# Kernel tuning notes

Measured on AMD Instinct MI355X. Metric: run time of the kernel, lower is better.

## Reference

```python
import jax, jax.numpy as jnp
import numpy as np

DIM = 384
HEADS = 6
K = 3  # kernel_size, stride = 1


def setup_inputs() -> dict:
    key = jax.random.key(0)
    ks = jax.random.split(key, 7)
    B, H, W, C = 16, 56, 56, DIM
    sc = 1.0 / np.sqrt(C)
    return {
        "x_map": jax.random.normal(ks[0], (B, H, W, C), dtype=jnp.float32),
        # Linear weights stored [in, out] (torch stores [out, in]; math identical)
        "W_attn": jax.random.normal(ks[1], (C, HEADS * K * K), dtype=jnp.float32) * sc,
        "b_attn": jax.random.normal(ks[2], (HEADS * K * K,), dtype=jnp.float32) * 0.02,
        "W_v": jax.random.normal(ks[3], (C, C), dtype=jnp.float32) * sc,
        "b_v": jax.random.normal(ks[4], (C,), dtype=jnp.float32) * 0.02,
        "W_proj": jax.random.normal(ks[5], (C, C), dtype=jnp.float32) * sc,
        "b_proj": jax.random.normal(ks[6], (C,), dtype=jnp.float32) * 0.02,
    }


def reference(x_map, W_attn, b_attn, W_v, b_v, W_proj, b_proj):
    B, H, W, C = x_map.shape
    k, heads = K, HEADS
    hd = C // heads
    pad = k // 2

    # attention logits per output pixel: [B, H*W, heads, k*k], softmax over window
    a = x_map @ W_attn + b_attn                     # [B,H,W,heads*k*k]
    a = jax.nn.softmax(a.reshape(B, H * W, heads, k * k), axis=-1)

    v = x_map @ W_v + b_v                           # [B,H,W,C]
    vp = jnp.pad(v, ((0, 0), (pad, pad), (pad, pad), (0, 0)))
    # k*k shifted views == F.unfold with row-major (ki,kj) kernel order
    patches = jnp.stack(
        [vp[:, i:i + H, j:j + W, :] for i in range(k) for j in range(k)],
        axis=3,
    )                                               # [B,H,W,k*k,C]
    patches = patches.reshape(B, H * W, k * k, heads, hd)

    # softmax-weighted sum over the k*k window, per head
    y = jnp.einsum('bpKhd,bphK->bphd', patches, a)  # [B,H*W,heads,hd]
    y = y.reshape(B, H, W, C)
    return y @ W_proj + b_proj
```

## Files before the change

### kernel.cpp

```cpp
#include <hip/hip_runtime.h>
#include <math.h>

#define NPIX 50176
#define CDIM 384
#define HEADS 6
#define NLOGIT 54
#define HH 56
#define WW 56
#define NCAT 448

typedef __attribute__((ext_vector_type(8))) __bf16 bf16x8;
typedef __attribute__((ext_vector_type(4))) float f32x4;

__device__ __forceinline__ void glds16(const void* g, void* l) {
  __builtin_amdgcn_global_load_lds(
      (const __attribute__((address_space(1))) unsigned int*)g,
      (__attribute__((address_space(3))) unsigned int*)l, 16, 0, 0);
}

__global__ __launch_bounds__(256) void prep_kernel(
    const float* __restrict__ W_v, const float* __restrict__ W_proj,
    const float* __restrict__ W_attn, const float* __restrict__ b_attn,
    __bf16* __restrict__ Wcat, __bf16* __restrict__ Wtp,
    float* __restrict__ bpad) {
  const int idx = blockIdx.x * 256 + threadIdx.x;
  const int CATSZ = NCAT * CDIM;
  const int WSZ   = CDIM * CDIM;
  if (idx < CATSZ) {
    const int n = idx / CDIM, k = idx % CDIM;
    float val;
    if (n < CDIM) val = W_v[k * CDIM + n];
    else {
      const int nn = n - CDIM;
      val = (nn < NLOGIT) ? W_attn[k * NLOGIT + nn] : 0.f;
    }
    Wcat[idx] = (__bf16)val;
  } else if (idx < CATSZ + WSZ) {
    const int r = idx - CATSZ;
    const int n = r / CDIM, k = r % CDIM;
    Wtp[r] = (__bf16)W_proj[k * CDIM + n];
  } else if (idx < CATSZ + WSZ + 64) {
    const int n = idx - CATSZ - WSZ;
    bpad[n] = (n < NLOGIT) ? b_attn[n] : 0.f;
  }
}

__global__ __launch_bounds__(256) void gemm_v_logit_kernel(
    const float* __restrict__ X, const __bf16* __restrict__ Wcat,
    const float* __restrict__ b_v, __bf16* __restrict__ v,
    const float* __restrict__ bpad, float* __restrict__ attn) {
  __shared__ char smem[33792];
  __bf16 (*As)[40] = (__bf16(*)[40])smem;
  __bf16 (*Bs)[32] = (__bf16(*)[32])(smem + 5120);
  float (*Ls)[68]  = (float(*)[68])smem;

  const int tid  = threadIdx.x;
  const int wave = tid >> 6;
  const int lane = tid & 63;
  const int bm   = blockIdx.x * 64;
  const int srow  = lane >> 2;
  const int skoff = (lane & 3) * 8;
  const int frow  = lane & 15;
  const int fk    = (lane >> 4) * 8;
  const size_t xrow = (size_t)(bm + wave * 16 + srow) * CDIM;

  f32x4 acc[28] = {};

  float4 pa0 = *(const float4*)(X + xrow + skoff);
  float4 pa1 = *(const float4*)(X + xrow + skoff + 4);

  for (int ks = 0; ks < 12; ++ks) {
    const int k0 = ks * 32;
    #pragma unroll
    for (int c = 0; c < 7; ++c) {
      const int brow = wave * 112 + c * 16;
      glds16(Wcat + (size_t)(brow + srow) * CDIM + k0 + skoff, &Bs[brow][0]);
    }
    bf16x8 h;
    h[0] = (__bf16)pa0.x; h[1] = (__bf16)pa0.y; h[2] = (__bf16)pa0.z; h[3] = (__bf16)pa0.w;
    h[4] = (__bf16)pa1.x; h[5] = (__bf16)pa1.y; h[6] = (__bf16)pa1.z; h[7] = (__bf16)pa1.w;
    *(bf16x8*)&As[wave * 16 + srow][skoff] = h;
    if (ks < 11) {
      pa0 = *(const float4*)(X + xrow + k0 + 32 + skoff);
      pa1 = *(const float4*)(X + xrow + k0 + 36 + skoff);
    }
    __syncthreads();

    const bf16x8 a = *(const bf16x8*)&As[wave * 16 + frow][fk];
    #pragma unroll
    for (int ni = 0; ni < 28; ++ni) {
      const bf16x8 b = *(const bf16x8*)&Bs[ni * 16 + frow][fk];
      acc[ni] = __builtin_amdgcn_mfma_f32_16x16x32_bf16(a, b, acc[ni], 0, 0, 0);
    }
    __syncthreads();
  }

  const int orow = (lane >> 4) * 4;

  #pragma unroll
  for (int ni = 0; ni < 24; ++ni) {
    const int n = ni * 16 + frow;
    const float bvl = b_v[n];
    #pragma unroll
    for (int r = 0; r < 4; ++r) {
      const int m = bm + wave * 16 + orow + r;
      v[(size_t)m * CDIM + n] = (__bf16)(acc[ni][r] + bvl);
    }
  }

  float bvl[4];
  #pragma unroll
  for (int ni = 0; ni < 4; ++ni) bvl[ni] = bpad[ni * 16 + frow];
  #pragma unroll
  for (int ni = 0; ni < 4; ++ni)
    #pragma unroll
    for (int r = 0; r < 4; ++r)
      Ls[wave * 16 + orow + r][ni * 16 + frow] = acc[24 + ni][r] + bvl[ni];
  __syncthreads();

  #pragma unroll
  for (int it = 0; it < 2; ++it) {
    const int task = it * 256 + tid;
    if (task < 64 * HEADS) {
      const int pl = task / HEADS;
      const int h  = task % HEADS;
      const float* row = &Ls[pl][h * 9];
      float m = row[0];
      #pragma unroll
      for (int w = 1; w < 9; ++w) m = fmaxf(m, row[w]);
      float e[9], s = 0.f;
      #pragma unroll
      for (int w = 0; w < 9; ++w) { e[w] = __expf(row[w] - m); s += e[w]; }
      const float inv = 1.f / s;
      float* op = &attn[(size_t)(bm + pl) * NLOGIT + h * 9];
      #pragma unroll
      for (int w = 0; w < 9; ++w) op[w] = e[w] * inv;
    }
  }
}

__global__ __launch_bounds__(256) void gemm_proj_kernel(
    const __bf16* __restrict__ A, const __bf16* __restrict__ Bt,
    const float* __restrict__ bias, float* __restrict__ Out) {
  __shared__ __bf16 As[64][32];
  __shared__ __bf16 Bs[384][32];

  const int tid  = threadIdx.x;
  const int wave = tid >> 6;
  const int lane = tid & 63;
  const int bm   = blockIdx.x * 64;
  const int srow  = lane >> 2;
  const int skoff = (lane & 3) * 8;
  const int frow  = lane & 15;
  const int fk    = (lane >> 4) * 8;

  f32x4 acc[24] = {};

  for (int ks = 0; ks < 12; ++ks) {
    const int k0 = ks * 32;
    glds16(A + (size_t)(bm + wave * 16 + srow) * CDIM + k0 + skoff,
           &As[wave * 16][0]);
    #pragma unroll
    for (int c = 0; c < 6; ++c) {
      const int brow = wave * 96 + c * 16;
      glds16(Bt + (size_t)(brow + srow) * CDIM + k0 + skoff, &Bs[brow][0]);
    }
    __syncthreads();

    const bf16x8 a = *(const bf16x8*)&As[wave * 16 + frow][fk];
    #pragma unroll
    for (int ni = 0; ni < 24; ++ni) {
      const bf16x8 b = *(const bf16x8*)&Bs[ni * 16 + frow][fk];
      acc[ni] = __builtin_amdgcn_mfma_f32_16x16x32_bf16(a, b, acc[ni], 0, 0, 0);
    }
    __syncthreads();
  }

  const int orow = (lane >> 4) * 4;
  #pragma unroll
  for (int ni = 0; ni < 24; ++ni) {
    const int n = ni * 16 + frow;
    const float bvl = bias[n];
    #pragma unroll
    for (int r = 0; r < 4; ++r) {
      const int m = bm + wave * 16 + orow + r;
      Out[(size_t)m * CDIM + n] = acc[ni][r] + bvl;
    }
  }
}

__global__ __launch_bounds__(256) void aggregate_kernel(
    const __bf16* __restrict__ v, const float* __restrict__ attn,
    __bf16* __restrict__ y) {
  const int idx = blockIdx.x * 256 + threadIdx.x;
  const int cg = idx % 48;
  const int pg = idx / 48;
  const int c  = cg * 8;
  const int b  = pg / ((HH / 4) * WW);
  const int r2 = pg % ((HH / 4) * WW);
  const int i0 = (r2 / WW) * 4;
  const int j  = r2 % WW;
  const int head = c >> 6;

  const int pbase = (b * HH + i0) * WW + j;
  float aw[4][9];
  #pragma unroll
  for (int p = 0; p < 4; ++p) {
    const float* ap = attn + (size_t)(pbase + p * WW) * NLOGIT + head * 9;
    #pragma unroll
    for (int w = 0; w < 9; ++w) aw[p][w] = ap[w];
  }

  const bool j0ok = (j > 0), j2ok = (j < WW - 1);
  float acc[4][8] = {};

  #pragma unroll
  for (int li = 0; li < 6; ++li) {
    const int ii = i0 - 1 + li;
    if (ii < 0 || ii >= HH) continue;
    const __bf16* vrow = v + ((size_t)(b * HH + ii) * WW + j) * CDIM + c;
    float ch[3][8];
    #pragma unroll
    for (int kj = 0; kj < 3; ++kj) {
      const bool ok = (kj == 0) ? j0ok : (kj == 2) ? j2ok : true;
      if (ok) {
        const bf16x8 vv = *(const bf16x8*)(vrow + (kj - 1) * CDIM);
        #pragma unroll
        for (int q = 0; q < 8; ++q) ch[kj][q] = (float)vv[q];
      } else {
        #pragma unroll
        for (int q = 0; q < 8; ++q) ch[kj][q] = 0.f;
      }
    }
    #pragma unroll
    for (int p = 0; p < 4; ++p) {
      const int ki = li - p;
      if (ki < 0 || ki > 2) continue;
      #pragma unroll
      for (int kj = 0; kj < 3; ++kj) {
        const float w = aw[p][ki * 3 + kj];
        #pragma unroll
        for (int q = 0; q < 8; ++q) acc[p][q] += w * ch[kj][q];
      }
    }
  }

  #pragma unroll
  for (int p = 0; p < 4; ++p) {
    bf16x8 o;
    #pragma unroll
    for (int q = 0; q < 8; ++q) o[q] = (__bf16)acc[p][q];
    *(bf16x8*)&y[(size_t)(pbase + p * WW) * CDIM + c] = o;
  }
}

extern "C" void kernel_launch(void* const* d_in, const int* in_sizes, int n_in,
                              void* d_out, int out_size, void* d_ws,
                              size_t ws_size, hipStream_t stream) {
  const float* x      = (const float*)d_in[0];
  const float* W_attn = (const float*)d_in[1];
  const float* b_attn = (const float*)d_in[2];
  const float* W_v    = (const float*)d_in[3];
  const float* b_v    = (const float*)d_in[4];
  const float* W_proj = (const float*)d_in[5];
  const float* b_proj = (const float*)d_in[6];
  float* out = (float*)d_out;

  char* w = (char*)d_ws;
  __bf16* v    = (__bf16*)w;  w += (size_t)NPIX * CDIM * 2;
  __bf16* y    = (__bf16*)w;  w += (size_t)NPIX * CDIM * 2;
  float*  attn = (float*)w;   w += (size_t)NPIX * NLOGIT * 4;
  __bf16* Wcat = (__bf16*)w;  w += (size_t)NCAT * CDIM * 2;
  __bf16* Wtp  = (__bf16*)w;  w += (size_t)CDIM * CDIM * 2;
  float*  bpad = (float*)w;   w += 64 * 4;

  const int prep_n = NCAT * CDIM + CDIM * CDIM + 64;
  prep_kernel<<<(prep_n + 255) / 256, 256, 0, stream>>>(
      W_v, W_proj, W_attn, b_attn, Wcat, Wtp, bpad);

  gemm_v_logit_kernel<<<NPIX / 64, 256, 0, stream>>>(
      x, Wcat, b_v, v, bpad, attn);

  aggregate_kernel<<<(NPIX / 4 * 48) / 256, 256, 0, stream>>>(v, attn, y);

  gemm_proj_kernel<<<NPIX / 64, 256, 0, stream>>>(y, Wtp, b_proj, out);
}
```

Measured before the change: 119.4 us.

## Pre-swizzle weights into MFMA fragment order and load A operands directly to registers

The prep kernel now writes both bf16 weight matrices in per-lane MFMA fragment order, so each k-step's B tile is a contiguous block copied straight into LDS and read back with linear, conflict-free 16-byte reads. The A operand (X or y) is loaded directly from global memory into registers in fragment layout, dropping the A shared-memory tile and its LDS round trip. The y load in the projection GEMM is prefetched one step ahead. The trade-off is that each lane's A loads now cover 16 distinct rows rather than coalesced row segments, which may reduce global coalescing.

Result: no change. 118.1 us (-1.1%).

```diff
diff --git a/kernel.cpp b/kernel.cpp
--- a/kernel.cpp
+++ b/kernel.cpp
@@ -8,6 +8,9 @@
 #define HH 56
 #define WW 56
 #define NCAT 448
+#define KSTEPS 12
+#define NCH_V 28
+#define NCH_P 24
 
 typedef __attribute__((ext_vector_type(8))) __bf16 bf16x8;
 typedef __attribute__((ext_vector_type(4))) float f32x4;
@@ -21,75 +24,90 @@
 __global__ __launch_bounds__(256) void prep_kernel(
     const float* __restrict__ W_v, const float* __restrict__ W_proj,
     const float* __restrict__ W_attn, const float* __restrict__ b_attn,
-    __bf16* __restrict__ Wcat, __bf16* __restrict__ Wtp,
+    __bf16* __restrict__ Wcat_frag, __bf16* __restrict__ Wtp_frag,
     float* __restrict__ bpad) {
-  const int idx = blockIdx.x * 256 + threadIdx.x;
-  const int CATSZ = NCAT * CDIM;
-  const int WSZ   = CDIM * CDIM;
-  if (idx < CATSZ) {
-    const int n = idx / CDIM, k = idx % CDIM;
-    float val;
-    if (n < CDIM) val = W_v[k * CDIM + n];
-    else {
-      const int nn = n - CDIM;
-      val = (nn < NLOGIT) ? W_attn[k * NLOGIT + nn] : 0.f;
-    }
-    Wcat[idx] = (__bf16)val;
-  } else if (idx < CATSZ + WSZ) {
-    const int r = idx - CATSZ;
-    const int n = r / CDIM, k = r % CDIM;
-    Wtp[r] = (__bf16)W_proj[k * CDIM + n];
-  } else if (idx < CATSZ + WSZ + 64) {
-    const int n = idx - CATSZ - WSZ;
+  const int gid = blockIdx.x * 256 + threadIdx.x;
+  const int NV = KSTEPS * NCH_V * 64;
+  const int NP = KSTEPS * NCH_P * 64;
+  if (gid < NV) {
+    const int ks   = gid / (NCH_V * 64);
+    const int rem  = gid % (NCH_V * 64);
+    const int ni   = rem >> 6;
+    const int lane = rem & 63;
+    const int n  = ni * 16 + (lane & 15);
+    const int kb = ks * 32 + (lane >> 4) * 8;
+    bf16x8 o;
+    #pragma unroll
+    for (int q = 0; q < 8; ++q) {
+      const int k = kb + q;
+      float val;
+      if (n < CDIM) val = W_v[k * CDIM + n];
+      else {
+        const int nn = n - CDIM;
+        val = (nn < NLOGIT) ? W_attn[k * NLOGIT + nn] : 0.f;
+      }
+      o[q] = (__bf16)val;
+    }
+    *(bf16x8*)&Wcat_frag[(size_t)gid * 8] = o;
+  } else if (gid < NV + NP) {
+    const int r    = gid - NV;
+    const int ks   = r / (NCH_P * 64);
+    const int rem  = r % (NCH_P * 64);
+    const int ni   = rem >> 6;
+    const int lane = rem & 63;
+    const int n  = ni * 16 + (lane & 15);
+    const int kb = ks * 32 + (lane >> 4) * 8;
+    bf16x8 o;
+    #pragma unroll
+    for (int q = 0; q < 8; ++q) o[q] = (__bf16)W_proj[(kb + q) * CDIM + n];
+    *(bf16x8*)&Wtp_frag[(size_t)r * 8] = o;
+  } else if (gid < NV + NP + 64) {
+    const int n = gid - NV - NP;
     bpad[n] = (n < NLOGIT) ? b_attn[n] : 0.f;
   }
 }
 
 __global__ __launch_bounds__(256) void gemm_v_logit_kernel(
-    const float* __restrict__ X, const __bf16* __restrict__ Wcat,
+    const float* __restrict__ X, const __bf16* __restrict__ Wcat_frag,
     const float* __restrict__ b_v, __bf16* __restrict__ v,
     const float* __restrict__ bpad, float* __restrict__ attn) {
-  __shared__ char smem[33792];
-  __bf16 (*As)[40] = (__bf16(*)[40])smem;
-  __bf16 (*Bs)[32] = (__bf16(*)[32])(smem + 5120);
-  float (*Ls)[68]  = (float(*)[68])smem;
+  __shared__ char smem[NCH_V * 1024];
+  __bf16* Bs = (__bf16*)smem;
+  float (*Ls)[68] = (float(*)[68])smem;
 
   const int tid  = threadIdx.x;
   const int wave = tid >> 6;
   const int lane = tid & 63;
   const int bm   = blockIdx.x * 64;
-  const int srow  = lane >> 2;
-  const int skoff = (lane & 3) * 8;
-  const int frow  = lane & 15;
-  const int fk    = (lane >> 4) * 8;
-  const size_t xrow = (size_t)(bm + wave * 16 + srow) * CDIM;
+  const int frow = lane & 15;
+  const int fk8  = (lane >> 4) * 8;
+
+  const int arow = bm + wave * 16 + frow;
+  const float* xrow = X + (size_t)arow * CDIM + fk8;
 
   f32x4 acc[28] = {};
-
-  float4 pa0 = *(const float4*)(X + xrow + skoff);
-  float4 pa1 = *(const float4*)(X + xrow + skoff + 4);
-
-  for (int ks = 0; ks < 12; ++ks) {
-    const int k0 = ks * 32;
+  float4 pa0 = *(const float4*)(xrow + 0);
+  float4 pa1 = *(const float4*)(xrow + 4);
+
+  for (int ks = 0; ks < KSTEPS; ++ks) {
     #pragma unroll
     for (int c = 0; c < 7; ++c) {
-      const int brow = wave * 112 + c * 16;
-      glds16(Wcat + (size_t)(brow + srow) * CDIM + k0 + skoff, &Bs[brow][0]);
-    }
-    bf16x8 h;
-    h[0] = (__bf16)pa0.x; h[1] = (__bf16)pa0.y; h[2] = (__bf16)pa0.z; h[3] = (__bf16)pa0.w;
-    h[4] = (__bf16)pa1.x; h[5] = (__bf16)pa1.y; h[6] = (__bf16)pa1.z; h[7] = (__bf16)pa1.w;
-    *(bf16x8*)&As[wave * 16 + srow][skoff] = h;
-    if (ks < 11) {
-      pa0 = *(const float4*)(X + xrow + k0 + 32 + skoff);
-      pa1 = *(const float4*)(X + xrow + k0 + 36 + skoff);
+      const int chunk = wave * 7 + c;
+      glds16(Wcat_frag + ((size_t)(ks * NCH_V + chunk) * 64 + lane) * 8,
+             Bs + chunk * 512);
+    }
+    bf16x8 a;
+    a[0] = (__bf16)pa0.x; a[1] = (__bf16)pa0.y; a[2] = (__bf16)pa0.z; a[3] = (__bf16)pa0.w;
+    a[4] = (__bf16)pa1.x; a[5] = (__bf16)pa1.y; a[6] = (__bf16)pa1.z; a[7] = (__bf16)pa1.w;
+    if (ks < KSTEPS - 1) {
+      pa0 = *(const float4*)(xrow + (ks + 1) * 32 + 0);
+      pa1 = *(const float4*)(xrow + (ks + 1) * 32 + 4);
     }
     __syncthreads();
 
-    const bf16x8 a = *(const bf16x8*)&As[wave * 16 + frow][fk];
     #pragma unroll
     for (int ni = 0; ni < 28; ++ni) {
-      const bf16x8 b = *(const bf16x8*)&Bs[ni * 16 + frow][fk];
+      const bf16x8 b = *(const bf16x8*)&Bs[(ni * 64 + lane) * 8];
       acc[ni] = __builtin_amdgcn_mfma_f32_16x16x32_bf16(a, b, acc[ni], 0, 0, 0);
     }
     __syncthreads();
@@ -140,40 +158,41 @@
 }
 
 __global__ __launch_bounds__(256) void gemm_proj_kernel(
-    const __bf16* __restrict__ A, const __bf16* __restrict__ Bt,
+    const __bf16* __restrict__ Y, const __bf16* __restrict__ Wtp_frag,
     const float* __restrict__ bias, float* __restrict__ Out) {
-  __shared__ __bf16 As[64][32];
-  __shared__ __bf16 Bs[384][32];
+  __shared__ __bf16 Bs[NCH_P * 512];
 
   const int tid  = threadIdx.x;
   const int wave = tid >> 6;
   const int lane = tid & 63;
   const int bm   = blockIdx.x * 64;
-  const int srow  = lane >> 2;
-  const int skoff = (lane & 3) * 8;
-  const int frow  = lane & 15;
-  const int fk    = (lane >> 4) * 8;
+  const int frow = lane & 15;
+  const int fk8  = (lane >> 4) * 8;
+
+  const int arow = bm + wave * 16 + frow;
+  const __bf16* yrow = Y + (size_t)arow * CDIM + fk8;
 
   f32x4 acc[24] = {};
-
-  for (int ks = 0; ks < 12; ++ks) {
-    const int k0 = ks * 32;
-    glds16(A + (size_t)(bm + wave * 16 + srow) * CDIM + k0 + skoff,
-           &As[wave * 16][0]);
+  bf16x8 a = *(const bf16x8*)(yrow);
+
+  for (int ks = 0; ks < KSTEPS; ++ks) {
     #pragma unroll
     for (int c = 0; c < 6; ++c) {
-      const int brow = wave * 96 + c * 16;
-      glds16(Bt + (size_t)(brow + srow) * CDIM + k0 + skoff, &Bs[brow][0]);
-    }
+      const int chunk = wave * 6 + c;
+      glds16(Wtp_frag + ((size_t)(ks * NCH_P + chunk) * 64 + lane) * 8,
+             Bs + chunk * 512);
+    }
+    bf16x8 a_next;
+    if (ks < KSTEPS - 1) a_next = *(const bf16x8*)(yrow + (ks + 1) * 32);
     __syncthreads();
 
-    const bf16x8 a = *(const bf16x8*)&As[wave * 16 + frow][fk];
     #pragma unroll
     for (int ni = 0; ni < 24; ++ni) {
-      const bf16x8 b = *(const bf16x8*)&Bs[ni * 16 + frow][fk];
+      const bf16x8 b = *(const bf16x8*)&Bs[(ni * 64 + lane) * 8];
       acc[ni] = __builtin_amdgcn_mfma_f32_16x16x32_bf16(a, b, acc[ni], 0, 0, 0);
     }
     __syncthreads();
+    a = a_next;
   }
 
   const int orow = (lane >> 4) * 4;
@@ -270,18 +289,18 @@
   __bf16* v    = (__bf16*)w;  w += (size_t)NPIX * CDIM * 2;
   __bf16* y    = (__bf16*)w;  w += (size_t)NPIX * CDIM * 2;
   float*  attn = (float*)w;   w += (size_t)NPIX * NLOGIT * 4;
-  __bf16* Wcat = (__bf16*)w;  w += (size_t)NCAT * CDIM * 2;
-  __bf16* Wtp  = (__bf16*)w;  w += (size_t)CDIM * CDIM * 2;
+  __bf16* Wcat_frag = (__bf16*)w;  w += (size_t)NCAT * CDIM * 2;
+  __bf16* Wtp_frag  = (__bf16*)w;  w += (size_t)CDIM * CDIM * 2;
   float*  bpad = (float*)w;   w += 64 * 4;
 
-  const int prep_n = NCAT * CDIM + CDIM * CDIM + 64;
+  const int prep_n = KSTEPS * NCH_V * 64 + KSTEPS * NCH_P * 64 + 64;
   prep_kernel<<<(prep_n + 255) / 256, 256, 0, stream>>>(
-      W_v, W_proj, W_attn, b_attn, Wcat, Wtp, bpad);
+      W_v, W_proj, W_attn, b_attn, Wcat_frag, Wtp_frag, bpad);
 
   gemm_v_logit_kernel<<<NPIX / 64, 256, 0, stream>>>(
-      x, Wcat, b_v, v, bpad, attn);
+      x, Wcat_frag, b_v, v, bpad, attn);
 
   aggregate_kernel<<<(NPIX / 4 * 48) / 256, 256, 0, stream>>>(v, attn, y);
 
-  gemm_proj_kernel<<<NPIX / 64, 256, 0, stream>>>(y, Wtp, b_proj, out);
-}
+  gemm_proj_kernel<<<NPIX / 64, 256, 0, stream>>>(y, Wtp_frag, b_proj, out);
+}
```
